# Optimization experiments

Hardware: AMD Instinct MI355X
Metric: run time of the kernel (lower is better)

## Reference

```python
import jax, jax.numpy as jnp
import numpy as np

DIM = 1024        # BIGNET_DIM
GROUP = 16        # Linear4Bit group_size
LORA = 20         # lora_dim hardcoded in Block
NLAYERS = 18      # 6 blocks * 3 QLoRALinear
NBLOCKS = 6
BATCH = 8192
EPS = 1e-5


def setup_inputs() -> dict:
    key = jax.random.key(0)
    ks = jax.random.split(key, 6)
    x = jax.random.normal(ks[0], (BATCH, DIM), jnp.float32)
    # int4 quantized base weights in [-8, 7], stored as int32
    qw = jax.random.randint(ks[1], (NLAYERS, DIM, DIM), -8, 8, jnp.int32)
    # per-(out_row, input-group) dequant scales
    scales = jax.random.uniform(ks[2], (NLAYERS, DIM, DIM // GROUP), jnp.float32,
                                minval=0.005, maxval=0.02)
    bias = jax.random.normal(ks[3], (NLAYERS, DIM), jnp.float32) * 0.01
    # lora_a: kaiming-uniform-like scale; lora_b: small nonzero (zeros in torch init,
    # randomized here so the LoRA path is numerically exercised)
    lora_a = jax.random.normal(ks[4], (NLAYERS, LORA, DIM), jnp.float32) / np.sqrt(DIM)
    lora_b = jax.random.normal(ks[5], (NLAYERS, DIM, LORA), jnp.float32) * 0.01
    ln_w = jnp.ones((NBLOCKS - 1, DIM), jnp.float32)
    ln_b = jnp.zeros((NBLOCKS - 1, DIM), jnp.float32)
    return dict(x=x, qw=qw, scales=scales, bias=bias,
                lora_a=lora_a, lora_b=lora_b, ln_w=ln_w, ln_b=ln_b)


def _qlora_linear(x, qw, sc, b, A, B):
    # dequantize: each group of 16 input cols of a row shares one scale
    w = (qw.astype(jnp.float32).reshape(DIM, DIM // GROUP, GROUP)
         * sc[:, :, None]).reshape(DIM, DIM)          # [out, in]
    base = x @ w.T + b                                # [N, out]
    lora = (x @ A.T) @ B.T                            # [N, r] @ [r, out]
    return base + lora


def _layernorm(x, w, b):
    m = jnp.mean(x, axis=-1, keepdims=True)
    v = jnp.mean((x - m) ** 2, axis=-1, keepdims=True)
    return (x - m) * jax.lax.rsqrt(v + EPS) * w + b


def reference(x, qw, scales, bias, lora_a, lora_b, ln_w, ln_b):
    h = x
    li = 0
    for blk in range(NBLOCKS):
        r = h
        for j in range(3):
            r = _qlora_linear(r, qw[li], scales[li], bias[li], lora_a[li], lora_b[li])
            if j < 2:
                r = jax.nn.relu(r)
            li += 1
        h = h + r  # residual
        if blk < NBLOCKS - 1:
            h = _layernorm(h, ln_w[blk], ln_b[blk])
    return h
```

## Files before the change

### kernel.cpp

```cpp
#include <hip/hip_runtime.h>
#include <cstdint>
#include <cstddef>

#define DIM      1024
#define GROUP    16
#define LORA     20
#define NLAYERS  18
#define NBLOCKS  6
#define BATCH    8192
#define EPS      1e-5f

typedef __bf16 bf16_8 __attribute__((ext_vector_type(8)));
typedef __bf16 bf16_4 __attribute__((ext_vector_type(4)));
typedef float  f32x4  __attribute__((ext_vector_type(4)));

__global__ __launch_bounds__(256, 2) void wprep_kernel(
    const int* __restrict__ qw, const float* __restrict__ sc,
    const float* __restrict__ la, const float* __restrict__ lb,
    __bf16* __restrict__ whi) {
  const int l  = blockIdx.x >> 7;
  const int og = (blockIdx.x >> 1) & 63;
  const int cg = blockIdx.x & 1;
  const int tid = threadIdx.x;

  __shared__ float As[10 * 512];
  __shared__ float Bs[16 * LORA];

  const float* Abase = la + (size_t)l * LORA * DIM + cg * 512;
  const float* Bbase = lb + ((size_t)l * DIM + og * 16) * LORA;
  for (int i = tid; i < 16 * LORA; i += 256) Bs[i] = Bbase[i];
#pragma unroll
  for (int i = 0; i < 5; ++i) {
    const int f4 = i * 256 + tid;
    ((float4*)As)[f4] = *(const float4*)(Abase + (size_t)(f4 >> 7) * DIM + (f4 & 127) * 4);
  }
  __syncthreads();

  const int tc = tid & 31;
  const int tr = tid >> 5;

  float acc[2][16];
  size_t rowb[2];
#pragma unroll
  for (int u = 0; u < 2; ++u) {
    const int orow = og * 16 + tr * 2 + u;
    rowb[u] = ((size_t)l * DIM + orow) * DIM + cg * 512;
    const size_t scb = ((size_t)l * DIM + orow) * (DIM / GROUP) + cg * 32;
#pragma unroll
    for (int v = 0; v < 4; ++v) {
      const int c = v * 128 + tc * 4;
      const int4 q4 = *(const int4*)&qw[rowb[u] + c];
      const float sv = sc[scb + (c >> 4)];
      acc[u][v * 4 + 0] = q4.x * sv;
      acc[u][v * 4 + 1] = q4.y * sv;
      acc[u][v * 4 + 2] = q4.z * sv;
      acc[u][v * 4 + 3] = q4.w * sv;
    }
  }

#pragma unroll 1
  for (int half = 0; half < 2; ++half) {
    if (half == 1) {
      __syncthreads();
#pragma unroll
      for (int i = 0; i < 5; ++i) {
        const int f4 = i * 256 + tid;
        ((float4*)As)[f4] =
            *(const float4*)(Abase + (size_t)(10 + (f4 >> 7)) * DIM + (f4 & 127) * 4);
      }
      __syncthreads();
    }
#pragma unroll 2
    for (int jj = 0; jj < 10; ++jj) {
      const int j = half * 10 + jj;
      float4 a[4];
#pragma unroll
      for (int v = 0; v < 4; ++v)
        a[v] = *(const float4*)&As[jj * 512 + v * 128 + tc * 4];
#pragma unroll
      for (int u = 0; u < 2; ++u) {
        const float bj = Bs[(tr * 2 + u) * LORA + j];
#pragma unroll
        for (int v = 0; v < 4; ++v) {
          acc[u][v * 4 + 0] += bj * a[v].x;
          acc[u][v * 4 + 1] += bj * a[v].y;
          acc[u][v * 4 + 2] += bj * a[v].z;
          acc[u][v * 4 + 3] += bj * a[v].w;
        }
      }
    }
  }

#pragma unroll
  for (int u = 0; u < 2; ++u) {
#pragma unroll
    for (int v = 0; v < 4; ++v) {
      const bf16_4 hv = {(__bf16)acc[u][v * 4 + 0], (__bf16)acc[u][v * 4 + 1],
                         (__bf16)acc[u][v * 4 + 2], (__bf16)acc[u][v * 4 + 3]};
      *(bf16_4*)&whi[rowb[u] + v * 128 + tc * 4] = hv;
    }
  }
}

__global__ __launch_bounds__(256) void xprep_kernel(
    const float* __restrict__ x, __bf16* __restrict__ hi) {
  const size_t i = (size_t)blockIdx.x * 256 + threadIdx.x;
  const float4 v = ((const float4*)x)[i];
  const bf16_4 hv = {(__bf16)v.x, (__bf16)v.y, (__bf16)v.z, (__bf16)v.w};
  ((bf16_4*)hi)[i] = hv;
}

#define GBUF    12288
#define GOFF_W  8192

template <int NISSUE>
__device__ __forceinline__ void stageR(const __bf16* __restrict__ g, int row0, int k0,
                                       __bf16* lds, int tid) {
#pragma unroll
  for (int i = 0; i < NISSUE; ++i) {
    const int D = i * 8192 + tid * 16;
    const int r  = D >> 6;
    const int ce = (D & 63) >> 1;
    const __bf16* gp = g + (size_t)(row0 + r) * DIM + k0 + ce;
    __builtin_amdgcn_global_load_lds(
        (const __attribute__((address_space(1))) void*)gp,
        (__attribute__((address_space(3))) void*)(lds + i * 4096 + (tid >> 6) * 512), 16, 0, 0);
  }
}

template <int MODE>
__global__ __launch_bounds__(512, 1) void gemm1_kernel(
    const __bf16* __restrict__ X, const __bf16* __restrict__ Wh,
    const float* __restrict__ bias, __bf16* __restrict__ Oh,
    const float* __restrict__ Hin,
    const float2* __restrict__ stats,
    const float* __restrict__ lnw, const float* __restrict__ lnb,
    float* __restrict__ Sout) {
  extern __shared__ __bf16 smem[];

  const int tid  = threadIdx.x;
  const int lane = tid & 63;
  const int wv   = tid >> 6;
  const int wm   = wv >> 2;
  const int wn2  = wv & 3;
  const int xcd = blockIdx.x & 7;
  const int kk  = blockIdx.x >> 3;
  const int tm  = xcd * 4 + (kk >> 3);
  const int tn  = kk & 7;
  const int rowX = tm * 256, rowW = tn * 128;

  const int lr   = lane & 15;
  const int slot = lane >> 4;

  int offX[4], offW[4];
#pragma unroll
  for (int n = 0; n < 4; ++n) offX[n] = (wn2 * 64 + n * 16 + lr) * 32 + slot * 8;
#pragma unroll
  for (int m = 0; m < 4; ++m) offW[m] = GOFF_W + (wm * 64 + m * 16 + lr) * 32 + slot * 8;

  f32x4 acc[4][4];
#pragma unroll
  for (int m = 0; m < 4; ++m)
#pragma unroll
    for (int n = 0; n < 4; ++n) acc[m][n] = f32x4{0.f, 0.f, 0.f, 0.f};

  auto stage_tile = [&](int t) {
    __bf16* sb = smem + (t % 6) * GBUF;
    stageR<2>(X,  rowX, t * 32, sb, tid);
    stageR<1>(Wh, rowW, t * 32, sb + GOFF_W, tid);
  };

  auto compute_tile = [&](int t) {
    const __bf16* buf = smem + (t % 6) * GBUF;
    bf16_8 xf[4];
#pragma unroll
    for (int n = 0; n < 4; ++n) xf[n] = *(const bf16_8*)&buf[offX[n]];
#pragma unroll
    for (int m = 0; m < 4; ++m) {
      const bf16_8 w_h = *(const bf16_8*)&buf[offW[m]];
#pragma unroll
      for (int n = 0; n < 4; ++n)
        acc[m][n] = __builtin_amdgcn_mfma_f32_16x16x32_bf16(w_h, xf[n], acc[m][n], 0, 0, 0);
    }
  };

  stage_tile(0); stage_tile(1); stage_tile(2); stage_tile(3);
  asm volatile("s_waitcnt vmcnt(6)" ::: "memory");
  __builtin_amdgcn_s_barrier();

#pragma unroll 1
  for (int kt = 0; kt < 28; kt += 2) {
    stage_tile(kt + 4);
    stage_tile(kt + 5);
    compute_tile(kt);
    compute_tile(kt + 1);
    asm volatile("s_waitcnt vmcnt(6)" ::: "memory");
    __builtin_amdgcn_s_barrier();
  }
  compute_tile(28);
  compute_tile(29);
  asm volatile("s_waitcnt vmcnt(0)" ::: "memory");
  __builtin_amdgcn_s_barrier();
  compute_tile(30);
  compute_tile(31);

  const int g4 = slot * 4;
#pragma unroll
  for (int m = 0; m < 4; ++m) {
    const int feat = tn * 128 + wm * 64 + m * 16 + g4;
    const float4 bv = *(const float4*)&bias[feat];
    float4 wq, bq;
    if constexpr (MODE == 2) {
      wq = *(const float4*)&lnw[feat];
      bq = *(const float4*)&lnb[feat];
    }
#pragma unroll
    for (int n = 0; n < 4; ++n) {
      const int nb = tm * 256 + wn2 * 64 + n * 16 + lr;
      const size_t base = (size_t)nb * DIM + feat;
      float v0 = acc[m][n][0] + bv.x;
      float v1 = acc[m][n][1] + bv.y;
      float v2 = acc[m][n][2] + bv.z;
      float v3 = acc[m][n][3] + bv.w;
      if constexpr (MODE == 0) {
        const bf16_4 hv = {(__bf16)fmaxf(v0, 0.f), (__bf16)fmaxf(v1, 0.f),
                           (__bf16)fmaxf(v2, 0.f), (__bf16)fmaxf(v3, 0.f)};
        *(bf16_4*)&Oh[base] = hv;
      } else if constexpr (MODE == 1) {
        const float4 h = *(const float4*)&Hin[base];
        *(float4*)&Sout[base] = float4{v0 + h.x, v1 + h.y, v2 + h.z, v3 + h.w};
      } else {
        const float2 st = stats[nb];
        const float4 s = *(const float4*)&Hin[base];
        const float h0 = (s.x - st.x) * st.y * wq.x + bq.x;
        const float h1 = (s.y - st.x) * st.y * wq.y + bq.y;
        const float h2 = (s.z - st.x) * st.y * wq.z + bq.z;
        const float h3 = (s.w - st.x) * st.y * wq.w + bq.w;
        *(float4*)&Sout[base] = float4{v0 + h0, v1 + h1, v2 + h2, v3 + h3};
      }
    }
  }
}

__global__ __launch_bounds__(256) void normcast_kernel(
    const float* __restrict__ S, const float* __restrict__ w,
    const float* __restrict__ b, float2* __restrict__ stats,
    __bf16* __restrict__ phi) {
  const int row = blockIdx.x;
  const int tid = threadIdx.x;
  const int lane = tid & 63;
  const int wv = tid >> 6;
  const float4 v = ((const float4*)(S + (size_t)row * DIM))[tid];

  float s = v.x + v.y + v.z + v.w;
#pragma unroll
  for (int m = 32; m; m >>= 1) s += __shfl_xor(s, m, 64);
  __shared__ float red[8];
  if (lane == 0) red[wv] = s;
  __syncthreads();
  const float mean = (red[0] + red[1] + red[2] + red[3]) * (1.f / DIM);

  const float d0 = v.x - mean, d1 = v.y - mean, d2 = v.z - mean, d3 = v.w - mean;
  float q = d0 * d0 + d1 * d1 + d2 * d2 + d3 * d3;
#pragma unroll
  for (int m = 32; m; m >>= 1) q += __shfl_xor(q, m, 64);
  if (lane == 0) red[4 + wv] = q;
  __syncthreads();
  const float var = (red[4] + red[5] + red[6] + red[7]) * (1.f / DIM);
  const float inv = 1.f / sqrtf(var + EPS);

  if (tid == 0) stats[row] = float2{mean, inv};

  const float4 wv4 = ((const float4*)w)[tid];
  const float4 bv4 = ((const float4*)b)[tid];
  const bf16_4 hv = {(__bf16)(d0 * inv * wv4.x + bv4.x),
                     (__bf16)(d1 * inv * wv4.y + bv4.y),
                     (__bf16)(d2 * inv * wv4.z + bv4.z),
                     (__bf16)(d3 * inv * wv4.w + bv4.w)};
  ((bf16_4*)phi)[(size_t)row * (DIM / 4) + tid] = hv;
}

extern "C" void kernel_launch(void* const* d_in, const int* in_sizes, int n_in,
                              void* d_out, int out_size, void* d_ws, size_t ws_size,
                              hipStream_t stream) {
  const float* x   = (const float*)d_in[0];
  const int*   qw  = (const int*)d_in[1];
  const float* sc  = (const float*)d_in[2];
  const float* bias= (const float*)d_in[3];
  const float* la  = (const float*)d_in[4];
  const float* lb  = (const float*)d_in[5];
  const float* lnw = (const float*)d_in[6];
  const float* lnb = (const float*)d_in[7];
  float* out = (float*)d_out;
  char* ws = (char*)d_ws;

  __bf16* WHI = (__bf16*)(ws);
  __bf16* X0  = (__bf16*)(ws + 37748736);
  __bf16* X1  = (__bf16*)(ws + 54525952);
  float*  SA  = (float*)(ws + 71303168);
  float*  SB  = (float*)(ws + 104857600);
  float2* STT = (float2*)(ws + 138412032);
  (void)ws_size; (void)in_sizes; (void)n_in; (void)out_size;

  xprep_kernel<<<BATCH * DIM / (256 * 4), 256, 0, stream>>>(x, X0);
  wprep_kernel<<<NLAYERS * 128, 256, 0, stream>>>(qw, sc, la, lb, WHI);

  const dim3 ggrid(BATCH / 256 * (DIM / 128));
  const size_t smem_bytes = 6 * GBUF * sizeof(__bf16);
  for (int blk = 0; blk < NBLOCKS; ++blk) {
    const int li = blk * 3;
    const size_t w0 = (size_t)li * DIM * DIM;
    const size_t w1 = (size_t)(li + 1) * DIM * DIM;
    const size_t w2 = (size_t)(li + 2) * DIM * DIM;
    float* Scur = (blk & 1) ? SB : SA;
    float* Sprev = (blk & 1) ? SA : SB;

    gemm1_kernel<0><<<ggrid, 512, smem_bytes, stream>>>(
        X0, WHI + w0, bias + (size_t)li * DIM, X1,
        nullptr, nullptr, nullptr, nullptr, nullptr);
    gemm1_kernel<0><<<ggrid, 512, smem_bytes, stream>>>(
        X1, WHI + w1, bias + (size_t)(li + 1) * DIM, X0,
        nullptr, nullptr, nullptr, nullptr, nullptr);
    float* sout = (blk == NBLOCKS - 1) ? out : Scur;
    if (blk == 0) {
      gemm1_kernel<1><<<ggrid, 512, smem_bytes, stream>>>(
          X0, WHI + w2, bias + (size_t)(li + 2) * DIM, nullptr,
          x, nullptr, nullptr, nullptr, sout);
    } else {
      gemm1_kernel<2><<<ggrid, 512, smem_bytes, stream>>>(
          X0, WHI + w2, bias + (size_t)(li + 2) * DIM, nullptr,
          Sprev, STT, lnw + (size_t)(blk - 1) * DIM, lnb + (size_t)(blk - 1) * DIM,
          sout);
    }
    if (blk < NBLOCKS - 1) {
      normcast_kernel<<<BATCH, 256, 0, stream>>>(
          Scur, lnw + (size_t)blk * DIM, lnb + (size_t)blk * DIM, STT, X0);
    }
  }
}
```

Baseline: 603.8 us.

## Shrink GEMM K-pipeline from six LDS buffers to three with single-tile steps

Restructures the GEMM main loop's LDS pipeline. It goes from six buffers, prefetching four tiles and stepping two tiles per barrier, to three static buffers that prefetch two tiles ahead and step one tile per barrier. The smaller static shared allocation cuts LDS footprint and may let more blocks co-reside, but it halves prefetch depth and doubles the number of barriers per K sweep, which could expose more memory latency.

```diff
diff --git a/kernel.cpp b/kernel.cpp
--- a/kernel.cpp
+++ b/kernel.cpp
@@ -136,7 +136,7 @@
     const float2* __restrict__ stats,
     const float* __restrict__ lnw, const float* __restrict__ lnb,
     float* __restrict__ Sout) {
-  extern __shared__ __bf16 smem[];
+  __shared__ __bf16 smem[3 * GBUF];
 
   const int tid  = threadIdx.x;
   const int lane = tid & 63;
@@ -164,14 +164,12 @@
 #pragma unroll
     for (int n = 0; n < 4; ++n) acc[m][n] = f32x4{0.f, 0.f, 0.f, 0.f};
 
-  auto stage_tile = [&](int t) {
-    __bf16* sb = smem + (t % 6) * GBUF;
-    stageR<2>(X,  rowX, t * 32, sb, tid);
-    stageR<1>(Wh, rowW, t * 32, sb + GOFF_W, tid);
+  auto stage_tile = [&](int k0, __bf16* sb) {
+    stageR<2>(X,  rowX, k0, sb, tid);
+    stageR<1>(Wh, rowW, k0, sb + GOFF_W, tid);
   };
 
-  auto compute_tile = [&](int t) {
-    const __bf16* buf = smem + (t % 6) * GBUF;
+  auto compute_tile = [&](const __bf16* buf) {
     bf16_8 xf[4];
 #pragma unroll
     for (int n = 0; n < 4; ++n) xf[n] = *(const bf16_8*)&buf[offX[n]];
@@ -184,25 +182,26 @@
     }
   };
 
-  stage_tile(0); stage_tile(1); stage_tile(2); stage_tile(3);
-  asm volatile("s_waitcnt vmcnt(6)" ::: "memory");
+  stage_tile(0, smem);
+  stage_tile(32, smem + GBUF);
+  asm volatile("s_waitcnt vmcnt(3)" ::: "memory");
   __builtin_amdgcn_s_barrier();
 
+  int cur = 0;
 #pragma unroll 1
-  for (int kt = 0; kt < 28; kt += 2) {
-    stage_tile(kt + 4);
-    stage_tile(kt + 5);
-    compute_tile(kt);
-    compute_tile(kt + 1);
-    asm volatile("s_waitcnt vmcnt(6)" ::: "memory");
+  for (int kt = 0; kt < 30; ++kt) {
+    int pb = cur + 2; if (pb >= 3) pb -= 3;
+    stage_tile((kt + 2) * 32, smem + pb * GBUF);
+    compute_tile(smem + cur * GBUF);
+    asm volatile("s_waitcnt vmcnt(3)" ::: "memory");
     __builtin_amdgcn_s_barrier();
-  }
-  compute_tile(28);
-  compute_tile(29);
+    ++cur; if (cur == 3) cur = 0;
+  }
+  compute_tile(smem + cur * GBUF);
   asm volatile("s_waitcnt vmcnt(0)" ::: "memory");
   __builtin_amdgcn_s_barrier();
-  compute_tile(30);
-  compute_tile(31);
+  ++cur; if (cur == 3) cur = 0;
+  compute_tile(smem + cur * GBUF);
 
   const int g4 = slot * 4;
 #pragma unroll
@@ -306,7 +305,6 @@
   wprep_kernel<<<NLAYERS * 128, 256, 0, stream>>>(qw, sc, la, lb, WHI);
 
   const dim3 ggrid(BATCH / 256 * (DIM / 128));
-  const size_t smem_bytes = 6 * GBUF * sizeof(__bf16);
   for (int blk = 0; blk < NBLOCKS; ++blk) {
     const int li = blk * 3;
     const size_t w0 = (size_t)li * DIM * DIM;
@@ -315,19 +313,19 @@
     float* Scur = (blk & 1) ? SB : SA;
     float* Sprev = (blk & 1) ? SA : SB;
 
-    gemm1_kernel<0><<<ggrid, 512, smem_bytes, stream>>>(
+    gemm1_kernel<0><<<ggrid, 512, 0, stream>>>(
         X0, WHI + w0, bias + (size_t)li * DIM, X1,
         nullptr, nullptr, nullptr, nullptr, nullptr);
-    gemm1_kernel<0><<<ggrid, 512, smem_bytes, stream>>>(
+    gemm1_kernel<0><<<ggrid, 512, 0, stream>>>(
         X1, WHI + w1, bias + (size_t)(li + 1) * DIM, X0,
         nullptr, nullptr, nullptr, nullptr, nullptr);
     float* sout = (blk == NBLOCKS - 1) ? out : Scur;
     if (blk == 0) {
-      gemm1_kernel<1><<<ggrid, 512, smem_bytes, stream>>>(
+      gemm1_kernel<1><<<ggrid, 512, 0, stream>>>(
           X0, WHI + w2, bias + (size_t)(li + 2) * DIM, nullptr,
           x, nullptr, nullptr, nullptr, sout);
     } else {
-      gemm1_kernel<2><<<ggrid, 512, smem_bytes, stream>>>(
+      gemm1_kernel<2><<<ggrid, 512, 0, stream>>>(
           X0, WHI + w2, bias + (size_t)(li + 2) * DIM, nullptr,
           Sprev, STT, lnw + (size_t)(blk - 1) * DIM, lnb + (size_t)(blk - 1) * DIM,
           sout);
```

Measured after the change: 577.2 us. 4.4% less time.

## Shrink GEMM LDS ring to four stages and hoist wprep weight loads

Applied to the files above, without the earlier changes.

The GEMM pipeline goes from a 6-buffer ring staging two tiles per iteration to a 4-buffer static LDS ring staging one tile per iteration three ahead, with adjusted waitcnt/barrier tail handling. This cuts LDS use, which may allow more occupancy or lower latency, but it adds a barrier per k-tile and shortens the prefetch distance. In wprep, the quantized weight and scale global loads are issued before the LoRA LDS staging so their latency overlaps, and the occupancy hint is raised to 3.

```diff
diff --git a/kernel.cpp b/kernel.cpp
--- a/kernel.cpp
+++ b/kernel.cpp
@@ -14,7 +14,7 @@
 typedef __bf16 bf16_4 __attribute__((ext_vector_type(4)));
 typedef float  f32x4  __attribute__((ext_vector_type(4)));
 
-__global__ __launch_bounds__(256, 2) void wprep_kernel(
+__global__ __launch_bounds__(256, 3) void wprep_kernel(
     const int* __restrict__ qw, const float* __restrict__ sc,
     const float* __restrict__ la, const float* __restrict__ lb,
     __bf16* __restrict__ whi) {
@@ -22,24 +22,11 @@
   const int og = (blockIdx.x >> 1) & 63;
   const int cg = blockIdx.x & 1;
   const int tid = threadIdx.x;
-
-  __shared__ float As[10 * 512];
-  __shared__ float Bs[16 * LORA];
-
-  const float* Abase = la + (size_t)l * LORA * DIM + cg * 512;
-  const float* Bbase = lb + ((size_t)l * DIM + og * 16) * LORA;
-  for (int i = tid; i < 16 * LORA; i += 256) Bs[i] = Bbase[i];
-#pragma unroll
-  for (int i = 0; i < 5; ++i) {
-    const int f4 = i * 256 + tid;
-    ((float4*)As)[f4] = *(const float4*)(Abase + (size_t)(f4 >> 7) * DIM + (f4 & 127) * 4);
-  }
-  __syncthreads();
-
   const int tc = tid & 31;
   const int tr = tid >> 5;
 
-  float acc[2][16];
+  int4  q[2][4];
+  float sv[2][4];
   size_t rowb[2];
 #pragma unroll
   for (int u = 0; u < 2; ++u) {
@@ -49,14 +36,34 @@
 #pragma unroll
     for (int v = 0; v < 4; ++v) {
       const int c = v * 128 + tc * 4;
-      const int4 q4 = *(const int4*)&qw[rowb[u] + c];
-      const float sv = sc[scb + (c >> 4)];
-      acc[u][v * 4 + 0] = q4.x * sv;
-      acc[u][v * 4 + 1] = q4.y * sv;
-      acc[u][v * 4 + 2] = q4.z * sv;
-      acc[u][v * 4 + 3] = q4.w * sv;
-    }
-  }
+      q[u][v] = *(const int4*)&qw[rowb[u] + c];
+      sv[u][v] = sc[scb + (c >> 4)];
+    }
+  }
+
+  __shared__ float As[10 * 512];
+  __shared__ float Bs[16 * LORA];
+
+  const float* Abase = la + (size_t)l * LORA * DIM + cg * 512;
+  const float* Bbase = lb + ((size_t)l * DIM + og * 16) * LORA;
+  for (int i = tid; i < 16 * LORA; i += 256) Bs[i] = Bbase[i];
+#pragma unroll
+  for (int i = 0; i < 5; ++i) {
+    const int f4 = i * 256 + tid;
+    ((float4*)As)[f4] = *(const float4*)(Abase + (size_t)(f4 >> 7) * DIM + (f4 & 127) * 4);
+  }
+  __syncthreads();
+
+  float acc[2][16];
+#pragma unroll
+  for (int u = 0; u < 2; ++u)
+#pragma unroll
+    for (int v = 0; v < 4; ++v) {
+      acc[u][v * 4 + 0] = q[u][v].x * sv[u][v];
+      acc[u][v * 4 + 1] = q[u][v].y * sv[u][v];
+      acc[u][v * 4 + 2] = q[u][v].z * sv[u][v];
+      acc[u][v * 4 + 3] = q[u][v].w * sv[u][v];
+    }
 
 #pragma unroll 1
   for (int half = 0; half < 2; ++half) {
@@ -136,7 +143,7 @@
     const float2* __restrict__ stats,
     const float* __restrict__ lnw, const float* __restrict__ lnb,
     float* __restrict__ Sout) {
-  extern __shared__ __bf16 smem[];
+  __shared__ __bf16 smem[4 * GBUF];
 
   const int tid  = threadIdx.x;
   const int lane = tid & 63;
@@ -165,13 +172,13 @@
     for (int n = 0; n < 4; ++n) acc[m][n] = f32x4{0.f, 0.f, 0.f, 0.f};
 
   auto stage_tile = [&](int t) {
-    __bf16* sb = smem + (t % 6) * GBUF;
+    __bf16* sb = smem + (t & 3) * GBUF;
     stageR<2>(X,  rowX, t * 32, sb, tid);
     stageR<1>(Wh, rowW, t * 32, sb + GOFF_W, tid);
   };
 
   auto compute_tile = [&](int t) {
-    const __bf16* buf = smem + (t % 6) * GBUF;
+    const __bf16* buf = smem + (t & 3) * GBUF;
     bf16_8 xf[4];
 #pragma unroll
     for (int n = 0; n < 4; ++n) xf[n] = *(const bf16_8*)&buf[offX[n]];
@@ -184,24 +191,23 @@
     }
   };
 
-  stage_tile(0); stage_tile(1); stage_tile(2); stage_tile(3);
+  stage_tile(0); stage_tile(1); stage_tile(2);
   asm volatile("s_waitcnt vmcnt(6)" ::: "memory");
   __builtin_amdgcn_s_barrier();
 
 #pragma unroll 1
-  for (int kt = 0; kt < 28; kt += 2) {
-    stage_tile(kt + 4);
-    stage_tile(kt + 5);
+  for (int kt = 0; kt < 29; ++kt) {
+    stage_tile(kt + 3);
     compute_tile(kt);
-    compute_tile(kt + 1);
     asm volatile("s_waitcnt vmcnt(6)" ::: "memory");
     __builtin_amdgcn_s_barrier();
   }
-  compute_tile(28);
   compute_tile(29);
+  asm volatile("s_waitcnt vmcnt(3)" ::: "memory");
+  __builtin_amdgcn_s_barrier();
+  compute_tile(30);
   asm volatile("s_waitcnt vmcnt(0)" ::: "memory");
   __builtin_amdgcn_s_barrier();
-  compute_tile(30);
   compute_tile(31);
 
   const int g4 = slot * 4;
@@ -306,7 +312,6 @@
   wprep_kernel<<<NLAYERS * 128, 256, 0, stream>>>(qw, sc, la, lb, WHI);
 
   const dim3 ggrid(BATCH / 256 * (DIM / 128));
-  const size_t smem_bytes = 6 * GBUF * sizeof(__bf16);
   for (int blk = 0; blk < NBLOCKS; ++blk) {
     const int li = blk * 3;
     const size_t w0 = (size_t)li * DIM * DIM;
@@ -315,19 +320,19 @@
     float* Scur = (blk & 1) ? SB : SA;
     float* Sprev = (blk & 1) ? SA : SB;
 
-    gemm1_kernel<0><<<ggrid, 512, smem_bytes, stream>>>(
+    gemm1_kernel<0><<<ggrid, 512, 0, stream>>>(
         X0, WHI + w0, bias + (size_t)li * DIM, X1,
         nullptr, nullptr, nullptr, nullptr, nullptr);
-    gemm1_kernel<0><<<ggrid, 512, smem_bytes, stream>>>(
+    gemm1_kernel<0><<<ggrid, 512, 0, stream>>>(
         X1, WHI + w1, bias + (size_t)(li + 1) * DIM, X0,
         nullptr, nullptr, nullptr, nullptr, nullptr);
     float* sout = (blk == NBLOCKS - 1) ? out : Scur;
     if (blk == 0) {
-      gemm1_kernel<1><<<ggrid, 512, smem_bytes, stream>>>(
+      gemm1_kernel<1><<<ggrid, 512, 0, stream>>>(
           X0, WHI + w2, bias + (size_t)(li + 2) * DIM, nullptr,
           x, nullptr, nullptr, nullptr, sout);
     } else {
-      gemm1_kernel<2><<<ggrid, 512, smem_bytes, stream>>>(
+      gemm1_kernel<2><<<ggrid, 512, 0, stream>>>(
           X0, WHI + w2, bias + (size_t)(li + 2) * DIM, nullptr,
           Sprev, STT, lnw + (size_t)(blk - 1) * DIM, lnb + (size_t)(blk - 1) * DIM,
           sout);
```

After: 553.7 us, median of 2. 1.09x faster.
